# Kernel optimization log

Hardware: AMD Instinct MI355X
Metric: run time of the kernel (lower is better)

## Reference

```python
import jax, jax.numpy as jnp
import numpy as np

B, S, D = 2, 2048, 1024
H, DH = 16, 64  # n_heads, d_head; D == H*DH
OUTPUT_SCALE = 1.0
EPS = 1e-08

def setup_inputs() -> dict:
    key = jax.random.key(0)
    k1, k2, k3 = jax.random.split(key, 3)
    x = jax.random.normal(k1, (B, S, D), dtype=jnp.float32)
    # causal-style mask would also work; use all-True [B,S,S] bool mask (True = attend)
    mask = jnp.tril(jnp.ones((S, S), dtype=bool))[None].repeat(B, axis=0)
    Wqkv = jax.random.normal(k2, (D, 3 * D), dtype=jnp.float32) * (1.0 / np.sqrt(D))
    Wo = jax.random.normal(k3, (D, D), dtype=jnp.float32) * (1.0 / np.sqrt(D))
    tau = jnp.full((H, 1, 1), float(DH) ** 0.5, dtype=jnp.float32)  # learned per-head temperature
    return {"x": x, "mask": mask, "Wqkv": Wqkv, "Wo": Wo, "tau": tau}

def reference(x, mask, Wqkv, Wo, tau):
    b, s, d = x.shape
    qkv = x @ Wqkv                                   # [B,S,3D]
    q, k, v = jnp.split(qkv, 3, axis=-1)
    # [B,S,D] -> [B,H,S,DH]
    q = q.reshape(b, s, H, DH).transpose(0, 2, 1, 3)
    k = k.reshape(b, s, H, DH).transpose(0, 2, 1, 3)
    v = v.reshape(b, s, H, DH).transpose(0, 2, 1, 3)
    # L2 normalize Q and K along head dim
    q = q / (jnp.linalg.norm(q, axis=-1, keepdims=True) + EPS)
    k = k / (jnp.linalg.norm(k, axis=-1, keepdims=True) + EPS)
    q = q * tau                                       # per-head learned temperature [H,1,1]
    logits = jnp.einsum('bhqd,bhkd->bhqk', q, k) / jnp.sqrt(jnp.float32(DH))
    m = mask if mask.ndim == 4 else mask[:, None, :, :]
    logits = jnp.where(m, logits, jnp.finfo(logits.dtype).min)
    w = jax.nn.softmax(logits, axis=-1)
    attn = jnp.einsum('bhqk,bhkd->bhqd', w, v)        # [B,H,S,DH]
    attn = attn.transpose(0, 2, 1, 3).reshape(b, s, d)
    return (attn @ Wo) * OUTPUT_SCALE
```

## Files before the change

kernel.cpp:

```cpp
#include <hip/hip_runtime.h>
#include <math.h>

#define BATCH 2
#define SEQ 2048
#define DMODEL 1024
#define NHEAD 16
#define DHEAD 64
#define QKV_COLS (3 * DMODEL)
#define EPS 1e-8f
#define LOG2E 1.44269504f

typedef short bf16x8 __attribute__((ext_vector_type(8)));
typedef float f32x4 __attribute__((ext_vector_type(4)));

static __device__ __forceinline__ unsigned short f2bf(float x) {
  unsigned u = __float_as_uint(x);
  u += 0x7fffu + ((u >> 16) & 1u);
  return (unsigned short)(u >> 16);
}

static __device__ __forceinline__ unsigned pkbf(float lo, float hi) {
  const unsigned ul = __float_as_uint(lo) + 0x8000u;
  const unsigned uh = __float_as_uint(hi) + 0x8000u;
  return __builtin_amdgcn_perm(uh, ul, 0x07060302);
}

static __device__ __forceinline__ void async_ld16(const unsigned short* g,
                                                  unsigned short* l) {
  __builtin_amdgcn_global_load_lds(
      (const __attribute__((address_space(1))) void*)g,
      (__attribute__((address_space(3))) void*)(unsigned int)(unsigned long long)l,
      16, 0, 0);
}

__global__ __launch_bounds__(256) void convert_x_kernel(
    const float* __restrict__ x, unsigned short* __restrict__ xb) {
  const size_t i = ((size_t)blockIdx.x * 256 + threadIdx.x) * 4;
  const float4 a = *(const float4*)(x + i);
  ushort4 r;
  r.x = f2bf(a.x); r.y = f2bf(a.y); r.z = f2bf(a.z); r.w = f2bf(a.w);
  *(ushort4*)(xb + i) = r;
}

__global__ __launch_bounds__(256) void transpose_w2_kernel(
    const float* __restrict__ W0, unsigned short* __restrict__ Wt0,
    const float* __restrict__ W1, unsigned short* __restrict__ Wt1) {
  __shared__ float tile[32][33];
  const int bx = blockIdx.x;
  const float* W;
  unsigned short* Wt;
  int N, n0;
  if (bx < 96) { W = W0; Wt = Wt0; N = QKV_COLS; n0 = bx * 32; }
  else         { W = W1; Wt = Wt1; N = DMODEL;   n0 = (bx - 96) * 32; }
  const int K = DMODEL;
  const int k0 = blockIdx.y * 32;
  const int tx = threadIdx.x, ty = threadIdx.y;
#pragma unroll
  for (int i = 0; i < 4; ++i)
    tile[ty + i * 8][tx] = W[(size_t)(k0 + ty + i * 8) * N + n0 + tx];
  __syncthreads();
#pragma unroll
  for (int i = 0; i < 4; ++i)
    Wt[(size_t)(n0 + ty + i * 8) * K + k0 + tx] = f2bf(tile[tx][ty + i * 8]);
}

__global__ __launch_bounds__(256) void sgemm_bf16_kernel(
    const unsigned short* __restrict__ A, const unsigned short* __restrict__ Bt,
    float* __restrict__ C, int M, int N, int K) {
  __shared__ unsigned short As[2][128 * 32];
  __shared__ unsigned short Bs[2][128 * 32];

  const int t = threadIdx.x;
  const int w = t >> 6;
  const int lane = t & 63;
  const int quad = lane >> 4;
  const int lr = lane & 15;
  const int wr = w >> 1, wc = w & 1;
  const int m0 = blockIdx.y * 128;
  const int n0 = blockIdx.x * 128;

  const int srow = w * 32 + (lane >> 2);
  const int scol = (lane & 3) * 8;
  const unsigned short* ga = A + (size_t)(m0 + srow) * K + scol;
  const unsigned short* gb = Bt + (size_t)(n0 + srow) * K + scol;

  auto stage = [&](int k0, int bb) {
#pragma unroll
    for (int i = 0; i < 2; ++i) {
      async_ld16(ga + (size_t)(i * 16) * K + k0, &As[bb][(w * 32 + i * 16) * 32]);
      async_ld16(gb + (size_t)(i * 16) * K + k0, &Bs[bb][(w * 32 + i * 16) * 32]);
    }
  };

  f32x4 acc[4][4];
  const f32x4 zero4 = {0.f, 0.f, 0.f, 0.f};
#pragma unroll
  for (int i = 0; i < 4; ++i)
#pragma unroll
    for (int j = 0; j < 4; ++j) acc[i][j] = zero4;

  stage(0, 0);
  int bb = 0;
  for (int k0 = 0; k0 < K; k0 += 32, bb ^= 1) {
    __syncthreads();
    if (k0 + 32 < K) stage(k0 + 32, bb ^ 1);

    bf16x8 af[4], bfr[4];
#pragma unroll
    for (int i = 0; i < 4; ++i)
      af[i] = *(const bf16x8*)&As[bb][(wr * 64 + i * 16 + lr) * 32 + quad * 8];
#pragma unroll
    for (int j = 0; j < 4; ++j)
      bfr[j] = *(const bf16x8*)&Bs[bb][(wc * 64 + j * 16 + lr) * 32 + quad * 8];
#pragma unroll
    for (int i = 0; i < 4; ++i)
#pragma unroll
      for (int j = 0; j < 4; ++j)
        acc[i][j] = __builtin_amdgcn_mfma_f32_16x16x32_bf16(af[i], bfr[j], acc[i][j], 0, 0, 0);
  }

#pragma unroll
  for (int i = 0; i < 4; ++i)
#pragma unroll
    for (int r = 0; r < 4; ++r) {
      float* c = C + (size_t)(m0 + wr * 64 + i * 16 + quad * 4 + r) * N + n0 + wc * 64 + lr;
#pragma unroll
      for (int j = 0; j < 4; ++j) c[j * 16] = acc[i][j][r];
    }
}

__global__ __launch_bounds__(256) void qkv_gemm_norm_kernel(
    const unsigned short* __restrict__ A, const unsigned short* __restrict__ Bt,
    const float* __restrict__ tau,
    unsigned short* __restrict__ Qh, unsigned short* __restrict__ Kh,
    unsigned short* __restrict__ Vh) {
  __shared__ unsigned short As[2][128 * 32];
  __shared__ unsigned short Bs[2][128 * 32];

  const int K = DMODEL, N = QKV_COLS;
  const int t = threadIdx.x;
  const int w = t >> 6;
  const int lane = t & 63;
  const int quad = lane >> 4;
  const int lr = lane & 15;
  const int wr = w >> 1, wc = w & 1;
  const int m0 = blockIdx.y * 128;
  const int n0 = blockIdx.x * 128;

  const int srow = w * 32 + (lane >> 2);
  const int scol = (lane & 3) * 8;
  const unsigned short* ga = A + (size_t)(m0 + srow) * K + scol;
  const unsigned short* gb = Bt + (size_t)(n0 + srow) * K + scol;

  auto stage = [&](int k0, int bb) {
#pragma unroll
    for (int i = 0; i < 2; ++i) {
      async_ld16(ga + (size_t)(i * 16) * K + k0, &As[bb][(w * 32 + i * 16) * 32]);
      async_ld16(gb + (size_t)(i * 16) * K + k0, &Bs[bb][(w * 32 + i * 16) * 32]);
    }
  };

  f32x4 acc[4][4];
  const f32x4 zero4 = {0.f, 0.f, 0.f, 0.f};
#pragma unroll
  for (int i = 0; i < 4; ++i)
#pragma unroll
    for (int j = 0; j < 4; ++j) acc[i][j] = zero4;

  stage(0, 0);
  int bb = 0;
  for (int k0 = 0; k0 < K; k0 += 32, bb ^= 1) {
    __syncthreads();
    if (k0 + 32 < K) stage(k0 + 32, bb ^ 1);

    bf16x8 af[4], bfr[4];
#pragma unroll
    for (int i = 0; i < 4; ++i)
      af[i] = *(const bf16x8*)&As[bb][(wr * 64 + i * 16 + lr) * 32 + quad * 8];
#pragma unroll
    for (int j = 0; j < 4; ++j)
      bfr[j] = *(const bf16x8*)&Bs[bb][(wc * 64 + j * 16 + lr) * 32 + quad * 8];
#pragma unroll
    for (int i = 0; i < 4; ++i)
#pragma unroll
      for (int j = 0; j < 4; ++j)
        acc[i][j] = __builtin_amdgcn_mfma_f32_16x16x32_bf16(af[i], bfr[j], acc[i][j], 0, 0, 0);
  }

  const int col0 = n0 + wc * 64;
  const int which = col0 >> 10;
  const int h = (col0 & 1023) >> 6;
  const float tsc = tau[h] * 0.125f * LOG2E;
  unsigned short* dst = (which == 0) ? Qh : (which == 1) ? Kh : Vh;

#pragma unroll
  for (int i = 0; i < 4; ++i)
#pragma unroll
    for (int r = 0; r < 4; ++r) {
      const int s = m0 + wr * 64 + i * 16 + quad * 4 + r;
      unsigned short* ar =
          dst + (((size_t)((s >> 11) * NHEAD + h)) * SEQ + (s & 2047)) * DHEAD;
      float scale;
      if (which == 2) {
        scale = 1.0f;
      } else {
        float ss = 0.f;
#pragma unroll
        for (int j = 0; j < 4; ++j) ss += acc[i][j][r] * acc[i][j][r];
        ss += __shfl_xor(ss, 1, 16);
        ss += __shfl_xor(ss, 2, 16);
        ss += __shfl_xor(ss, 4, 16);
        ss += __shfl_xor(ss, 8, 16);
        scale = 1.0f / (sqrtf(ss) + EPS);
        if (which == 0) scale *= tsc;
      }
#pragma unroll
      for (int j = 0; j < 4; ++j) ar[j * 16 + lr] = f2bf(acc[i][j][r] * scale);
    }
}

__global__ __launch_bounds__(256) void vtrans_kernel(
    const unsigned short* __restrict__ Vh, unsigned short* __restrict__ Vt) {
  __shared__ unsigned short tile[64][72];
  const int bh = blockIdx.x;
  const int s0 = blockIdx.y * 64;
  const int t = threadIdx.x;
  const int sr = t >> 2;
  const int dc = (t & 3) * 16;
  const unsigned short* src = Vh + ((size_t)bh * SEQ + s0 + sr) * DHEAD + dc;
  *(bf16x8*)&tile[sr][dc]     = *(const bf16x8*)(src);
  *(bf16x8*)&tile[sr][dc + 8] = *(const bf16x8*)(src + 8);
  __syncthreads();
  const int dr = t >> 2;
  const int sc = (t & 3) * 16;
  unsigned short buf[16];
#pragma unroll
  for (int i = 0; i < 16; ++i) buf[i] = tile[sc + i][dr];
  unsigned short* dst = Vt + ((size_t)bh * DHEAD + dr) * SEQ + s0 + sc;
  *(bf16x8*)dst       = *(const bf16x8*)buf;
  *(bf16x8*)(dst + 8) = *(const bf16x8*)(buf + 8);
}

__global__ __launch_bounds__(256, 4) void attn_kernel(
    const unsigned short* __restrict__ Qh, const unsigned short* __restrict__ Kh,
    const unsigned short* __restrict__ Vt, unsigned short* __restrict__ attnb) {
  __shared__ unsigned short Ks[2][64 * 64];
  __shared__ unsigned short Vs[2][64 * 64];

  const int idx = blockIdx.x;
  const int bh = idx & 31;
  const int i2 = idx >> 5;
  const int seg = i2 >> 3, G = i2 & 7;
  const int qb = (seg == 0) ? 31 - G : (seg == 1) ? G : (seg == 2) ? 23 - G : 8 + G;
  const int b = bh >> 4;
  const int h = bh & 15;
  const int t = threadIdx.x;
  const int w = t >> 6;
  const int lane = t & 63;
  const int quad = lane >> 4;
  const int lr = lane & 15;
  const int sw = lr & 7;

  const unsigned short* Qp = Qh + (size_t)bh * SEQ * DHEAD;
  const unsigned short* Kp = Kh + (size_t)bh * SEQ * DHEAD;
  const unsigned short* Vp = Vt + (size_t)bh * DHEAD * SEQ;

  const int rrow = lane >> 3;
  const int swc = ((lane & 7) ^ rrow) * 8;
  const int f0 = w * 4;

  auto stage = [&](int k0, int bb) {
#pragma unroll
    for (int ii = 0; ii < 4; ++ii) {
      const int fi = f0 + ii;
      if (fi < 8) {
        async_ld16(Kp + (size_t)(k0 + fi * 8 + rrow) * DHEAD + swc,
                   &Ks[bb][fi * 512]);
      } else {
        const int g = fi - 8;
        async_ld16(Vp + (size_t)(g * 8 + rrow) * SEQ + k0 + swc,
                   &Vs[bb][g * 512]);
      }
    }
  };

  const f32x4 zero4 = {0.f, 0.f, 0.f, 0.f};
  f32x4 o[4];
  o[0] = o[1] = o[2] = o[3] = zero4;
  float l_ = 0.f;

  const int q0 = qb * 64 + w * 16;
  const unsigned short* qr = Qp + (size_t)(q0 + lr) * DHEAD;
  const bf16x8 aq0 = *(const bf16x8*)(qr + quad * 8);
  const bf16x8 aq1 = *(const bf16x8*)(qr + 32 + quad * 8);
  const int qrow = q0 + lr;

  const int kend = qb * 64;

  stage(0, 0);
  int bb = 0;

  for (int k0 = 0; k0 <= kend; k0 += 64, bb ^= 1) {
    __syncthreads();
    if (k0 < kend) stage(k0 + 64, bb ^ 1);

    f32x4 c[4];
    __builtin_amdgcn_s_setprio(1);
#pragma unroll
    for (int kt = 0; kt < 4; ++kt) {
      const bf16x8 kf0 =
          *(const bf16x8*)&Ks[bb][(kt * 16 + lr) * 64 + ((quad ^ sw) * 8)];
      const bf16x8 kf1 =
          *(const bf16x8*)&Ks[bb][(kt * 16 + lr) * 64 + (((4 | quad) ^ sw) * 8)];
      f32x4 tt = __builtin_amdgcn_mfma_f32_16x16x32_bf16(kf0, aq0, zero4, 0, 0, 0);
      c[kt] = __builtin_amdgcn_mfma_f32_16x16x32_bf16(kf1, aq1, tt, 0, 0, 0);
    }
    __builtin_amdgcn_s_setprio(0);

    unsigned plo[4], phi[4];
    float ps = 0.f;
    if (k0 == kend) {
#pragma unroll
      for (int kt = 0; kt < 4; ++kt) {
        float p[4];
#pragma unroll
        for (int r = 0; r < 4; ++r) {
          const int key = k0 + kt * 16 + quad * 4 + r;
          p[r] = (key <= qrow) ? exp2f(c[kt][r]) : 0.f;
          ps += p[r];
        }
        plo[kt] = pkbf(p[0], p[1]);
        phi[kt] = pkbf(p[2], p[3]);
      }
    } else {
#pragma unroll
      for (int kt = 0; kt < 4; ++kt) {
        float p[4];
#pragma unroll
        for (int r = 0; r < 4; ++r) {
          p[r] = exp2f(c[kt][r]);
          ps += p[r];
        }
        plo[kt] = pkbf(p[0], p[1]);
        phi[kt] = pkbf(p[2], p[3]);
      }
    }
    l_ += ps;

#pragma unroll
    for (int c2 = 0; c2 < 2; ++c2) {
      unsigned aLo = plo[2 * c2],     aHi = phi[2 * c2];
      unsigned bLo = plo[2 * c2 + 1], bHi = phi[2 * c2 + 1];
      asm("v_permlane32_swap_b32 %0, %1" : "+v"(aLo), "+v"(bLo));
      asm("v_permlane32_swap_b32 %0, %1" : "+v"(aHi), "+v"(bHi));
      asm("v_permlane16_swap_b32 %0, %1" : "+v"(aLo), "+v"(bLo));
      asm("v_permlane16_swap_b32 %0, %1" : "+v"(aHi), "+v"(bHi));
      union { unsigned u[4]; bf16x8 v; } pk;
      pk.u[0] = aLo; pk.u[1] = aHi; pk.u[2] = bLo; pk.u[3] = bHi;
      const bf16x8 pa = pk.v;
      __builtin_amdgcn_s_setprio(1);
#pragma unroll
      for (int nt = 0; nt < 4; ++nt) {
        const bf16x8 vb = *(const bf16x8*)&Vs[bb][(nt * 16 + lr) * 64 +
                                                  (((c2 * 4 + quad) ^ sw) * 8)];
        o[nt] = __builtin_amdgcn_mfma_f32_16x16x32_bf16(pa, vb, o[nt], 0, 0, 0);
      }
      __builtin_amdgcn_s_setprio(0);
    }
  }

  float lt = l_;
  lt += __shfl_xor(lt, 16, 64);
  lt += __shfl_xor(lt, 32, 64);
  const float inv = 1.0f / lt;
#pragma unroll
  for (int r = 0; r < 4; ++r) {
    const float invr = __shfl(inv, quad * 4 + r, 16);
    unsigned short* ar =
        attnb + ((size_t)(b * SEQ + q0 + quad * 4 + r)) * DMODEL + h * DHEAD;
#pragma unroll
    for (int nt = 0; nt < 4; ++nt) ar[nt * 16 + lr] = f2bf(o[nt][r] * invr);
  }
}

extern "C" void kernel_launch(void* const* d_in, const int* in_sizes, int n_in,
                              void* d_out, int out_size, void* d_ws, size_t ws_size,
                              hipStream_t stream) {
  const float* x    = (const float*)d_in[0];
  const float* Wqkv = (const float*)d_in[2];
  const float* Wo   = (const float*)d_in[3];
  const float* tau  = (const float*)d_in[4];
  float* out = (float*)d_out;

  unsigned short* attnb = (unsigned short*)d_ws;
  unsigned short* Qh = attnb + (size_t)BATCH * SEQ * DMODEL;
  unsigned short* Kh = Qh + (size_t)BATCH * NHEAD * SEQ * DHEAD;
  unsigned short* Vh = Kh + (size_t)BATCH * NHEAD * SEQ * DHEAD;
  unsigned short* Xb = Vh + (size_t)BATCH * NHEAD * SEQ * DHEAD;
  unsigned short* Wqkv_t = Xb + (size_t)BATCH * SEQ * DMODEL;
  unsigned short* Wo_t = Wqkv_t + (size_t)DMODEL * QKV_COLS;
  unsigned short* Vt = Wo_t + (size_t)DMODEL * DMODEL;

  const int M = BATCH * SEQ;

  convert_x_kernel<<<(M * DMODEL) / (256 * 4), 256, 0, stream>>>(x, Xb);
  transpose_w2_kernel<<<dim3(128, 32), dim3(32, 8), 0, stream>>>(
      Wqkv, Wqkv_t, Wo, Wo_t);

  qkv_gemm_norm_kernel<<<dim3(QKV_COLS / 128, M / 128), 256, 0, stream>>>(
      Xb, Wqkv_t, tau, Qh, Kh, Vh);

  vtrans_kernel<<<dim3(BATCH * NHEAD, SEQ / 64), 256, 0, stream>>>(Vh, Vt);

  attn_kernel<<<dim3(1024), 256, 0, stream>>>(Qh, Kh, Vt, attnb);

  sgemm_bf16_kernel<<<dim3(DMODEL / 128, M / 128), 256, 0, stream>>>(
      attnb, Wo_t, out, M, DMODEL, DMODEL);
}
```

Measured before the change: 199.7 us.

## Restructure QKV GEMM into 256x256 tiles with swizzled LDS and phased pipelining

The QKV projection GEMM moves from 128x128 tiles with a 32-wide K step and 4 waves to 256x256 tiles with a 64-wide K step and 8 waves. Shared memory is XOR-swizzled to avoid bank conflicts. Each K step is split into four quarter phases that interleave async global loads with MFMA work, using explicit vmcnt waits, barriers and setprio. This cuts global traffic per FLOP and per-iteration sync overhead, at the cost of 128KB of LDS per block and only 192 blocks, which may underfill the GPU.

Result: slower. 205.7 us (+3.0%).

```diff
diff --git a/kernel.cpp b/kernel.cpp
--- a/kernel.cpp
+++ b/kernel.cpp
@@ -129,63 +129,113 @@
     }
 }
 
-__global__ __launch_bounds__(256) void qkv_gemm_norm_kernel(
+__global__ __launch_bounds__(512, 2) void qkv_gemm_norm_kernel(
     const unsigned short* __restrict__ A, const unsigned short* __restrict__ Bt,
     const float* __restrict__ tau,
     unsigned short* __restrict__ Qh, unsigned short* __restrict__ Kh,
     unsigned short* __restrict__ Vh) {
-  __shared__ unsigned short As[2][128 * 32];
-  __shared__ unsigned short Bs[2][128 * 32];
-
-  const int K = DMODEL, N = QKV_COLS;
+  __shared__ unsigned short As[2][256 * 64];
+  __shared__ unsigned short Bs[2][256 * 64];
+
+  const int K = DMODEL;
   const int t = threadIdx.x;
   const int w = t >> 6;
   const int lane = t & 63;
   const int quad = lane >> 4;
   const int lr = lane & 15;
-  const int wr = w >> 1, wc = w & 1;
-  const int m0 = blockIdx.y * 128;
-  const int n0 = blockIdx.x * 128;
-
-  const int srow = w * 32 + (lane >> 2);
-  const int scol = (lane & 3) * 8;
-  const unsigned short* ga = A + (size_t)(m0 + srow) * K + scol;
-  const unsigned short* gb = Bt + (size_t)(n0 + srow) * K + scol;
-
-  auto stage = [&](int k0, int bb) {
-#pragma unroll
-    for (int i = 0; i < 2; ++i) {
-      async_ld16(ga + (size_t)(i * 16) * K + k0, &As[bb][(w * 32 + i * 16) * 32]);
-      async_ld16(gb + (size_t)(i * 16) * K + k0, &Bs[bb][(w * 32 + i * 16) * 32]);
+  const int wr = w >> 2;
+  const int wc = w & 3;
+  const int m0 = blockIdx.y * 256;
+  const int n0 = blockIdx.x * 256;
+  const int swz = lr & 7;
+
+  const int rrow = lane >> 3;
+  const int swc = ((lane & 7) ^ rrow) * 8;
+
+  auto stA = [&](int k0, int bb, int hi) {
+#pragma unroll
+    for (int j = 0; j < 2; ++j) {
+      const int L = w * 16 + j * 8;
+      const int row = hi * 64 + L + (L & 64);
+      async_ld16(A + (size_t)(m0 + row + rrow) * K + k0 + swc, &As[bb][row * 64]);
     }
   };
-
-  f32x4 acc[4][4];
+  auto stB = [&](int k0, int bb, int hi) {
+#pragma unroll
+    for (int j = 0; j < 2; ++j) {
+      const int L = w * 16 + j * 8;
+      const int row = ((L & ~31) << 1) + (L & 31) + hi * 32;
+      async_ld16(Bt + (size_t)(n0 + row + rrow) * K + k0 + swc, &Bs[bb][row * 64]);
+    }
+  };
+
+  f32x4 acc[8][4];
   const f32x4 zero4 = {0.f, 0.f, 0.f, 0.f};
 #pragma unroll
-  for (int i = 0; i < 4; ++i)
+  for (int i = 0; i < 8; ++i)
 #pragma unroll
     for (int j = 0; j < 4; ++j) acc[i][j] = zero4;
 
-  stage(0, 0);
-  int bb = 0;
-  for (int k0 = 0; k0 < K; k0 += 32, bb ^= 1) {
-    __syncthreads();
-    if (k0 + 32 < K) stage(k0 + 32, bb ^ 1);
-
-    bf16x8 af[4], bfr[4];
-#pragma unroll
-    for (int i = 0; i < 4; ++i)
-      af[i] = *(const bf16x8*)&As[bb][(wr * 64 + i * 16 + lr) * 32 + quad * 8];
-#pragma unroll
-    for (int j = 0; j < 4; ++j)
-      bfr[j] = *(const bf16x8*)&Bs[bb][(wc * 64 + j * 16 + lr) * 32 + quad * 8];
-#pragma unroll
-    for (int i = 0; i < 4; ++i)
-#pragma unroll
-      for (int j = 0; j < 4; ++j)
-        acc[i][j] = __builtin_amdgcn_mfma_f32_16x16x32_bf16(af[i], bfr[j], acc[i][j], 0, 0, 0);
-  }
+#define PHASE(bb_, mB_, nB_, STAGEBODY, WAITBODY)                              \
+  {                                                                            \
+    bf16x8 af[4][2], bq[2][2];                                                 \
+    _Pragma("unroll")                                                          \
+    for (int m2 = 0; m2 < 4; ++m2)                                             \
+      _Pragma("unroll")                                                        \
+      for (int kk = 0; kk < 2; ++kk)                                           \
+        af[m2][kk] = *(const bf16x8*)&As[bb_][                                 \
+            (wr * 128 + ((mB_) * 4 + m2) * 16 + lr) * 64 +                     \
+            (((kk * 4 + quad) ^ swz) * 8)];                                    \
+    _Pragma("unroll")                                                          \
+    for (int n2 = 0; n2 < 2; ++n2)                                             \
+      _Pragma("unroll")                                                        \
+      for (int kk = 0; kk < 2; ++kk)                                           \
+        bq[n2][kk] = *(const bf16x8*)&Bs[bb_][                                 \
+            (wc * 64 + ((nB_) * 2 + n2) * 16 + lr) * 64 +                      \
+            (((kk * 4 + quad) ^ swz) * 8)];                                    \
+    STAGEBODY;                                                                 \
+    WAITBODY;                                                                  \
+    __builtin_amdgcn_s_setprio(1);                                             \
+    _Pragma("unroll")                                                          \
+    for (int m2 = 0; m2 < 4; ++m2)                                             \
+      _Pragma("unroll")                                                        \
+      for (int n2 = 0; n2 < 2; ++n2)                                           \
+        _Pragma("unroll")                                                      \
+        for (int kk = 0; kk < 2; ++kk)                                         \
+          acc[(mB_) * 4 + m2][(nB_) * 2 + n2] =                                \
+              __builtin_amdgcn_mfma_f32_16x16x32_bf16(                         \
+                  af[m2][kk], bq[n2][kk], acc[(mB_) * 4 + m2][(nB_) * 2 + n2], \
+                  0, 0, 0);                                                    \
+    __builtin_amdgcn_s_setprio(0);                                             \
+    __builtin_amdgcn_s_barrier();                                              \
+  }
+
+#define WAIT4 asm volatile("s_waitcnt vmcnt(4)\ns_barrier" ::: "memory")
+#define WAIT2 asm volatile("s_waitcnt vmcnt(2)\ns_barrier" ::: "memory")
+#define WAIT0 asm volatile("s_waitcnt vmcnt(0)\ns_barrier" ::: "memory")
+#define WAITB asm volatile("s_barrier" ::: "memory")
+#define NOSTAGE ((void)0)
+
+  stA(0, 0, 0); stB(0, 0, 0); stB(0, 0, 1); stA(0, 0, 1);
+  WAIT4;
+
+  const int NT = K / 64;
+  for (int tt = 0; tt < NT - 1; ++tt) {
+    const int bb = tt & 1, nb = bb ^ 1;
+    const int k0n = (tt + 1) * 64;
+    PHASE(bb, 0, 0, stA(k0n, nb, 0), WAIT4);
+    PHASE(bb, 0, 1, stB(k0n, nb, 0), WAIT4);
+    PHASE(bb, 1, 0, stB(k0n, nb, 1), WAIT4);
+    PHASE(bb, 1, 1, stA(k0n, nb, 1), WAIT4);
+  }
+  {
+    const int bb = (NT - 1) & 1;
+    PHASE(bb, 0, 0, NOSTAGE, WAIT2);
+    PHASE(bb, 0, 1, NOSTAGE, WAIT0);
+    PHASE(bb, 1, 0, NOSTAGE, WAITB);
+    PHASE(bb, 1, 1, NOSTAGE, WAITB);
+  }
+#undef PHASE
 
   const int col0 = n0 + wc * 64;
   const int which = col0 >> 10;
@@ -194,10 +244,10 @@
   unsigned short* dst = (which == 0) ? Qh : (which == 1) ? Kh : Vh;
 
 #pragma unroll
-  for (int i = 0; i < 4; ++i)
+  for (int m = 0; m < 8; ++m)
 #pragma unroll
     for (int r = 0; r < 4; ++r) {
-      const int s = m0 + wr * 64 + i * 16 + quad * 4 + r;
+      const int s = m0 + wr * 128 + m * 16 + quad * 4 + r;
       unsigned short* ar =
           dst + (((size_t)((s >> 11) * NHEAD + h)) * SEQ + (s & 2047)) * DHEAD;
       float scale;
@@ -206,7 +256,7 @@
       } else {
         float ss = 0.f;
 #pragma unroll
-        for (int j = 0; j < 4; ++j) ss += acc[i][j][r] * acc[i][j][r];
+        for (int n = 0; n < 4; ++n) ss += acc[m][n][r] * acc[m][n][r];
         ss += __shfl_xor(ss, 1, 16);
         ss += __shfl_xor(ss, 2, 16);
         ss += __shfl_xor(ss, 4, 16);
@@ -215,7 +265,7 @@
         if (which == 0) scale *= tsc;
       }
 #pragma unroll
-      for (int j = 0; j < 4; ++j) ar[j * 16 + lr] = f2bf(acc[i][j][r] * scale);
+      for (int n = 0; n < 4; ++n) ar[n * 16 + lr] = f2bf(acc[m][n][r] * scale);
     }
 }
 
@@ -407,7 +457,7 @@
   transpose_w2_kernel<<<dim3(128, 32), dim3(32, 8), 0, stream>>>(
       Wqkv, Wqkv_t, Wo, Wo_t);
 
-  qkv_gemm_norm_kernel<<<dim3(QKV_COLS / 128, M / 128), 256, 0, stream>>>(
+  qkv_gemm_norm_kernel<<<dim3(QKV_COLS / 256, M / 256), 512, 0, stream>>>(
       Xb, Wqkv_t, tau, Qh, Kh, Vh);
 
   vtrans_kernel<<<dim3(BATCH * NHEAD, SEQ / 64), 256, 0, stream>>>(Vh, Vt);
```
